# Kernel tuning notes

Hardware: AMD Instinct MI355X
Metric: run time of the kernel (lower is better)

The kernel has to match this reference:

```python
import jax, jax.numpy as jnp
import numpy as np


def setup_inputs() -> dict:
    key = jax.random.key(0)
    k1, k2, k3, k4, k5 = jax.random.split(key, 5)
    B, N, C = 16, 131072, 2
    return {
        "r": jax.random.normal(k1, (B, N, C), dtype=jnp.float32),
        "w": jax.random.uniform(k2, (B, N, 2), dtype=jnp.float32),
        "J_p": jax.random.normal(k3, (B, N, C, 6), dtype=jnp.float32),
        "J_d": jax.random.normal(k4, (B, N, C, 1), dtype=jnp.float32),
        "lmbda": jax.random.uniform(k5, (B, 1, 1), dtype=jnp.float32),
        "iter_idx": 1,
    }


def reference(r, w, J_p, J_d, lmbda, iter_idx):
    B, N, C = r.shape
    eye6 = jnp.eye(6, dtype=r.dtype)

    safe_lmbda = jnp.where(jnp.isnan(lmbda), jnp.asarray(100.0, r.dtype), lmbda)
    safe_lmbda = jnp.maximum(safe_lmbda, 0.001)  # (B,1,1)

    conf = w[..., 0:1][..., None]                 # (B,N,1,1)
    node_lambda = w[..., 1:2]                     # (B,N,1)
    cJp = conf * J_p                              # (B,N,C,6)
    cJd = conf * J_d                              # (B,N,C,1)
    cr = w[..., 0:1] * r                          # (B,N,C)

    H_pp = jnp.einsum('bncp,bncq->bpq', J_p, cJp)            # (B,6,6)
    H_pd = jnp.einsum('bncp,bncd->bnpd', J_p, cJd)           # (B,N,6,1)
    H_dd = jnp.sum(J_d * cJd, axis=2)                        # (B,N,1)
    g_p = jnp.einsum('bncp,bnc->bp', J_p, cr)[..., None]     # (B,6,1)
    g_d = jnp.sum(J_d * cr[..., None], axis=2)               # (B,N,1)

    H_pp = H_pp + safe_lmbda * eye6[None]
    H_dd_safe = jnp.maximum(H_dd + safe_lmbda + node_lambda + 1e-4, 1e-4)
    inv_H_dd = 1.0 / H_dd_safe                    # (B,N,1)

    H_pd_invHdd = H_pd * inv_H_dd[..., None]      # (B,N,6,1)
    term_to_sub = jnp.einsum('bnpd,bnqd->bpq', H_pd_invHdd, H_pd)   # (B,6,6)
    H_eff = H_pp - term_to_sub
    g_eff = g_p - jnp.sum(H_pd_invHdd * g_d[..., None], axis=1)     # (B,6,1)

    if iter_idx >= 2:
        g_eff = g_eff.at[:, 3:].set(0.0)
        H_eff = H_eff.at[:, 3:, 3:].add(1e8)

    H_eff = H_eff + 1.0 * eye6[None]
    diag = jnp.diagonal(H_eff, axis1=-2, axis2=-1)            # (B,6)
    H_eff = H_eff + eye6[None] * (0.01 * diag)[:, :, None]

    delta_pose = jnp.linalg.solve(H_eff, g_eff)               # (B,6,1)
    v = jnp.einsum('bnpd,bp->bnd', H_pd, delta_pose[..., 0])  # (B,N,1)
    delta_depth = inv_H_dd * (g_d - v)                        # (B,N,1)

    delta_pose = jnp.clip(delta_pose[..., 0], -2.0, 2.0)      # (B,6)
    delta_depth = jnp.clip(delta_depth, -5.0, 5.0)
    delta_pose = jnp.where(jnp.any(jnp.isnan(delta_pose)), jnp.zeros_like(delta_pose), delta_pose)
    delta_depth = jnp.where(jnp.any(jnp.isnan(delta_depth)), jnp.zeros_like(delta_depth), delta_depth)
    return (delta_pose, delta_depth)
```

## Files before the change

kernel.cpp:

```cpp
#include <hip/hip_runtime.h>
#include <math.h>

#define BATCH 16
#define NPB 131072
#define BLOCKS_PER_B 64
#define THREADS 256
#define PPT (NPB / (BLOCKS_PER_B * THREADS))
#define NACC 27

__device__ __forceinline__ float safe_lambda(float l) {
    if (isnan(l)) l = 100.0f;
    return fmaxf(l, 0.001f);
}

struct Pt { float4 a0, a1, a2; float2 jd, rv, wv; };

__device__ __forceinline__ void load_pt(const float* __restrict__ Jp, const float* __restrict__ Jd,
                                        const float* __restrict__ r, const float* __restrict__ w,
                                        long n, Pt& P)
{
    const float4* jp4 = (const float4*)(Jp + n * 12);
    P.a0 = jp4[0]; P.a1 = jp4[1]; P.a2 = jp4[2];
    P.jd = *(const float2*)(Jd + n * 2);
    P.rv = *(const float2*)(r  + n * 2);
    P.wv = *(const float2*)(w  + n * 2);
}

__device__ __forceinline__ void acc_pt(const Pt& P, float lam, float (&D)[21], float (&G)[6])
{
    float jp[12] = {P.a0.x, P.a0.y, P.a0.z, P.a0.w,
                    P.a1.x, P.a1.y, P.a1.z, P.a1.w,
                    P.a2.x, P.a2.y, P.a2.z, P.a2.w};
    const float conf = P.wv.x, nl = P.wv.y;
    const float jdx = P.jd.x, jdy = P.jd.y;
    const float rx  = P.rv.x, ry  = P.rv.y;

    float cjp[12];
#pragma unroll
    for (int i = 0; i < 12; ++i) cjp[i] = conf * jp[i];

    float h[6], hi[6];
#pragma unroll
    for (int p = 0; p < 6; ++p) h[p] = cjp[p] * jdx + cjp[6 + p] * jdy;
    const float Hdd = conf * (jdx * jdx + jdy * jdy);
    const float gd  = conf * (jdx * rx + jdy * ry);
    const float inv = 1.0f / fmaxf(Hdd + lam + nl + 1e-4f, 1e-4f);
#pragma unroll
    for (int p = 0; p < 6; ++p) hi[p] = h[p] * inv;

    int idx = 0;
#pragma unroll
    for (int p = 0; p < 6; ++p) {
#pragma unroll
        for (int q = p; q < 6; ++q) {
            D[idx] += cjp[p] * jp[q];
            D[idx] += cjp[6 + p] * jp[6 + q];
            D[idx] -= hi[p] * h[q];
            ++idx;
        }
    }
#pragma unroll
    for (int p = 0; p < 6; ++p) {
        G[p] += cjp[p] * rx;
        G[p] += cjp[6 + p] * ry;
        G[p] -= hi[p] * gd;
    }
}

__global__ __launch_bounds__(THREADS, 2) void dba_pass1(
    const float* __restrict__ r, const float* __restrict__ w,
    const float* __restrict__ Jp, const float* __restrict__ Jd,
    const float* __restrict__ lmbda, float* __restrict__ partials)
{
    const int b   = blockIdx.y;
    const int blk = blockIdx.x;
    const int t   = threadIdx.x;
    const float lam = safe_lambda(lmbda[b]);

    float D[21], G[6];
#pragma unroll
    for (int i = 0; i < 21; ++i) D[i] = 0.0f;
#pragma unroll
    for (int i = 0; i < 6; ++i) G[i] = 0.0f;

    const long base = (long)b * NPB + (long)blk * (THREADS * PPT) + t;

    Pt P0, P1, P2, P3;
    load_pt(Jp, Jd, r, w, base + 0 * THREADS, P0);
    load_pt(Jp, Jd, r, w, base + 1 * THREADS, P1);
    load_pt(Jp, Jd, r, w, base + 2 * THREADS, P2);

    acc_pt(P0, lam, D, G); load_pt(Jp, Jd, r, w, base + 3 * THREADS, P3);
    acc_pt(P1, lam, D, G); load_pt(Jp, Jd, r, w, base + 4 * THREADS, P0);
    acc_pt(P2, lam, D, G); load_pt(Jp, Jd, r, w, base + 5 * THREADS, P1);
    acc_pt(P3, lam, D, G); load_pt(Jp, Jd, r, w, base + 6 * THREADS, P2);
    acc_pt(P0, lam, D, G); load_pt(Jp, Jd, r, w, base + 7 * THREADS, P3);
    acc_pt(P1, lam, D, G);
    acc_pt(P2, lam, D, G);
    acc_pt(P3, lam, D, G);

#pragma unroll
    for (int i = 0; i < 21; ++i) {
        float v = D[i];
        v += __shfl_xor(v, 1);  v += __shfl_xor(v, 2);  v += __shfl_xor(v, 4);
        v += __shfl_xor(v, 8);  v += __shfl_xor(v, 16); v += __shfl_xor(v, 32);
        D[i] = v;
    }
#pragma unroll
    for (int i = 0; i < 6; ++i) {
        float v = G[i];
        v += __shfl_xor(v, 1);  v += __shfl_xor(v, 2);  v += __shfl_xor(v, 4);
        v += __shfl_xor(v, 8);  v += __shfl_xor(v, 16); v += __shfl_xor(v, 32);
        G[i] = v;
    }

    __shared__ float s_red[4][NACC];
    const int wid  = t >> 6;
    const int lane = t & 63;
    if (lane == 0) {
#pragma unroll
        for (int i = 0; i < 21; ++i) s_red[wid][i] = D[i];
#pragma unroll
        for (int i = 0; i < 6; ++i)  s_red[wid][21 + i] = G[i];
    }
    __syncthreads();
    if (t < NACC) {
        float v = s_red[0][t] + s_red[1][t] + s_red[2][t] + s_red[3][t];
        partials[((long)b * NACC + t) * BLOCKS_PER_B + blk] = v;
    }
}

__global__ void dba_solve(
    const float* __restrict__ partials, const float* __restrict__ lmbda,
    const int* __restrict__ iter_idx,
    float* __restrict__ out_pose,
    float* __restrict__ dp_raw)
{
    const int b = blockIdx.x;
    const int t = threadIdx.x;
    __shared__ float s[NACC];
    if (t < NACC) {
        const float4* p4 = (const float4*)(partials + ((long)b * NACC + t) * BLOCKS_PER_B);
        float4 a = make_float4(0.f, 0.f, 0.f, 0.f);
#pragma unroll
        for (int k = 0; k < BLOCKS_PER_B / 4; ++k) {
            float4 v = p4[k];
            a.x += v.x; a.y += v.y; a.z += v.z; a.w += v.w;
        }
        s[t] = (a.x + a.y) + (a.z + a.w);
    }
    __syncthreads();
    if (t != 0) return;

    const float lam = safe_lambda(lmbda[b]);
    float H[6][6], g[6];
    int idx = 0;
    for (int p = 0; p < 6; ++p)
        for (int q = p; q < 6; ++q) {
            float v = s[idx];
            H[p][q] = v; H[q][p] = v;
            idx++;
        }
    for (int p = 0; p < 6; ++p) g[p] = s[21 + p];
    for (int p = 0; p < 6; ++p) H[p][p] += lam;

    if (*iter_idx >= 2) {
        for (int p = 3; p < 6; ++p) g[p] = 0.0f;
        for (int p = 3; p < 6; ++p)
            for (int q = 3; q < 6; ++q) H[p][q] += 1e8f;
    }
    for (int p = 0; p < 6; ++p) H[p][p] += 1.0f;
    for (int p = 0; p < 6; ++p) H[p][p] += 0.01f * H[p][p];

    float A[6][7];
    for (int p = 0; p < 6; ++p) {
        for (int q = 0; q < 6; ++q) A[p][q] = H[p][q];
        A[p][6] = g[p];
    }
    for (int col = 0; col < 6; ++col) {
        int piv = col; float best = fabsf(A[col][col]);
        for (int rr = col + 1; rr < 6; ++rr) {
            float v = fabsf(A[rr][col]);
            if (v > best) { best = v; piv = rr; }
        }
        if (piv != col)
            for (int cc = col; cc < 7; ++cc) {
                float tmp = A[col][cc]; A[col][cc] = A[piv][cc]; A[piv][cc] = tmp;
            }
        const float invp = 1.0f / A[col][col];
        for (int rr = col + 1; rr < 6; ++rr) {
            const float f = A[rr][col] * invp;
            for (int cc = col; cc < 7; ++cc) A[rr][cc] -= f * A[col][cc];
        }
    }
    float x[6];
    for (int rr = 5; rr >= 0; --rr) {
        float v = A[rr][6];
        for (int cc = rr + 1; cc < 6; ++cc) v -= A[rr][cc] * x[cc];
        x[rr] = v / A[rr][rr];
    }
    for (int p = 0; p < 6; ++p) {
        dp_raw[b * 6 + p] = x[p];
        out_pose[b * 6 + p] = fminf(fmaxf(x[p], -2.0f), 2.0f);
    }
}

__device__ __forceinline__ float depth_pt(const Pt& P, float lam, const float (&dp)[6])
{
    float jp[12] = {P.a0.x, P.a0.y, P.a0.z, P.a0.w,
                    P.a1.x, P.a1.y, P.a1.z, P.a1.w,
                    P.a2.x, P.a2.y, P.a2.z, P.a2.w};
    const float conf = P.wv.x, nl = P.wv.y;
    const float jdx = P.jd.x, jdy = P.jd.y;
    const float rx  = P.rv.x, ry  = P.rv.y;

    float v = 0.0f;
#pragma unroll
    for (int p = 0; p < 6; ++p) {
        const float h = conf * (jp[p] * jdx + jp[6 + p] * jdy);
        v += h * dp[p];
    }
    const float Hdd = conf * (jdx * jdx + jdy * jdy);
    const float gd  = conf * (jdx * rx + jdy * ry);
    const float inv = 1.0f / fmaxf(Hdd + lam + nl + 1e-4f, 1e-4f);
    float dd = inv * (gd - v);
    return fminf(fmaxf(dd, -5.0f), 5.0f);
}

__global__ __launch_bounds__(THREADS, 2) void dba_pass3(
    const float* __restrict__ r, const float* __restrict__ w,
    const float* __restrict__ Jp, const float* __restrict__ Jd,
    const float* __restrict__ lmbda, const float* __restrict__ dp_raw,
    float* __restrict__ out_dd)
{
    const int b   = blockIdx.y;
    const int blk = blockIdx.x;
    const int t   = threadIdx.x;
    const float lam = safe_lambda(lmbda[b]);

    float dp[6];
#pragma unroll
    for (int p = 0; p < 6; ++p) dp[p] = dp_raw[b * 6 + p];

    const long base = (long)b * NPB + (long)blk * (THREADS * PPT) + t;

    Pt P0, P1, P2, P3;
    load_pt(Jp, Jd, r, w, base + 0 * THREADS, P0);
    load_pt(Jp, Jd, r, w, base + 1 * THREADS, P1);
    load_pt(Jp, Jd, r, w, base + 2 * THREADS, P2);

    out_dd[base + 0 * THREADS] = depth_pt(P0, lam, dp); load_pt(Jp, Jd, r, w, base + 3 * THREADS, P3);
    out_dd[base + 1 * THREADS] = depth_pt(P1, lam, dp); load_pt(Jp, Jd, r, w, base + 4 * THREADS, P0);
    out_dd[base + 2 * THREADS] = depth_pt(P2, lam, dp); load_pt(Jp, Jd, r, w, base + 5 * THREADS, P1);
    out_dd[base + 3 * THREADS] = depth_pt(P3, lam, dp); load_pt(Jp, Jd, r, w, base + 6 * THREADS, P2);
    out_dd[base + 4 * THREADS] = depth_pt(P0, lam, dp); load_pt(Jp, Jd, r, w, base + 7 * THREADS, P3);
    out_dd[base + 5 * THREADS] = depth_pt(P1, lam, dp);
    out_dd[base + 6 * THREADS] = depth_pt(P2, lam, dp);
    out_dd[base + 7 * THREADS] = depth_pt(P3, lam, dp);
}

extern "C" void kernel_launch(void* const* d_in, const int* in_sizes, int n_in,
                              void* d_out, int out_size, void* d_ws, size_t ws_size,
                              hipStream_t stream) {
    const float* r     = (const float*)d_in[0];
    const float* w     = (const float*)d_in[1];
    const float* Jp    = (const float*)d_in[2];
    const float* Jd    = (const float*)d_in[3];
    const float* lmbda = (const float*)d_in[4];
    const int*   iter  = (const int*)  d_in[5];

    float* out      = (float*)d_out;
    float* partials = (float*)d_ws;
    float* dp_raw   = partials + (long)BATCH * NACC * BLOCKS_PER_B;

    dim3 grid(BLOCKS_PER_B, BATCH);
    dba_pass1<<<grid, THREADS, 0, stream>>>(r, w, Jp, Jd, lmbda, partials);
    dba_solve<<<BATCH, 64, 0, stream>>>(partials, lmbda, iter, out, dp_raw);
    dba_pass3<<<grid, THREADS, 0, stream>>>(r, w, Jp, Jd, lmbda, dp_raw, out + BATCH * 6);
}
```

Baseline: 60.64 us.

## Stage J_p through LDS with global_load_lds in both streaming passes

Both the reduction pass and the depth pass now copy each wave's 64-point J_p chunk into LDS using the direct global-to-LDS load builtin with coalesced 16-byte lanes. Each thread then reads its 12 floats back from LDS. This replaces the per-thread strided float4 loads and the hand-unrolled four-deep register prefetch with a simple loop that waits on vmcnt(0) every iteration. The aim is more coalesced J_p traffic, at the cost of losing cross-iteration load overlap and adding an LDS round trip.

Result: no change. 61.52 us (+1.4%).

```diff
diff --git a/kernel.cpp b/kernel.cpp
--- a/kernel.cpp
+++ b/kernel.cpp
@@ -5,6 +5,7 @@
 #define NPB 131072
 #define BLOCKS_PER_B 64
 #define THREADS 256
+#define NWAVE (THREADS / 64)
 #define PPT (NPB / (BLOCKS_PER_B * THREADS))
 #define NACC 27
 
@@ -13,27 +14,29 @@
     return fmaxf(l, 0.001f);
 }
 
-struct Pt { float4 a0, a1, a2; float2 jd, rv, wv; };
-
-__device__ __forceinline__ void load_pt(const float* __restrict__ Jp, const float* __restrict__ Jd,
-                                        const float* __restrict__ r, const float* __restrict__ w,
-                                        long n, Pt& P)
-{
-    const float4* jp4 = (const float4*)(Jp + n * 12);
-    P.a0 = jp4[0]; P.a1 = jp4[1]; P.a2 = jp4[2];
-    P.jd = *(const float2*)(Jd + n * 2);
-    P.rv = *(const float2*)(r  + n * 2);
-    P.wv = *(const float2*)(w  + n * 2);
-}
-
-__device__ __forceinline__ void acc_pt(const Pt& P, float lam, float (&D)[21], float (&G)[6])
-{
-    float jp[12] = {P.a0.x, P.a0.y, P.a0.z, P.a0.w,
-                    P.a1.x, P.a1.y, P.a1.z, P.a1.w,
-                    P.a2.x, P.a2.y, P.a2.z, P.a2.w};
-    const float conf = P.wv.x, nl = P.wv.y;
-    const float jdx = P.jd.x, jdy = P.jd.y;
-    const float rx  = P.rv.x, ry  = P.rv.y;
+__device__ __forceinline__ void gload_lds16(const float* g, float* l) {
+    __builtin_amdgcn_global_load_lds(
+        (const __attribute__((address_space(1))) void*)g,
+        (__attribute__((address_space(3))) void*)l, 16, 0, 0);
+}
+
+__device__ __forceinline__ void stage_jp(const float* __restrict__ Jp, long wave_pt,
+                                         float* lds_slice, int lane) {
+    const float* src = Jp + wave_pt * 12 + (long)lane * 4;
+    gload_lds16(src,       lds_slice);
+    gload_lds16(src + 256, lds_slice + 256);
+    gload_lds16(src + 512, lds_slice + 512);
+}
+
+__device__ __forceinline__ void acc_pt_lds(const float* jp_lane, float2 jd, float2 rv, float2 wv,
+                                           float lam, float (&D)[21], float (&G)[6])
+{
+    const float4* f4 = (const float4*)jp_lane;
+    float4 a0 = f4[0], a1 = f4[1], a2 = f4[2];
+    float jp[12] = {a0.x, a0.y, a0.z, a0.w, a1.x, a1.y, a1.z, a1.w, a2.x, a2.y, a2.z, a2.w};
+    const float conf = wv.x, nl = wv.y;
+    const float jdx = jd.x, jdy = jd.y;
+    const float rx  = rv.x, ry  = rv.y;
 
     float cjp[12];
 #pragma unroll
@@ -72,32 +75,37 @@
     const float* __restrict__ Jp, const float* __restrict__ Jd,
     const float* __restrict__ lmbda, float* __restrict__ partials)
 {
-    const int b   = blockIdx.y;
-    const int blk = blockIdx.x;
-    const int t   = threadIdx.x;
+    const int b    = blockIdx.y;
+    const int blk  = blockIdx.x;
+    const int t    = threadIdx.x;
+    const int wid  = t >> 6;
+    const int lane = t & 63;
     const float lam = safe_lambda(lmbda[b]);
 
+    __shared__ float lds_jp[NWAVE][768];
+
     float D[21], G[6];
 #pragma unroll
     for (int i = 0; i < 21; ++i) D[i] = 0.0f;
 #pragma unroll
     for (int i = 0; i < 6; ++i) G[i] = 0.0f;
 
-    const long base = (long)b * NPB + (long)blk * (THREADS * PPT) + t;
-
-    Pt P0, P1, P2, P3;
-    load_pt(Jp, Jd, r, w, base + 0 * THREADS, P0);
-    load_pt(Jp, Jd, r, w, base + 1 * THREADS, P1);
-    load_pt(Jp, Jd, r, w, base + 2 * THREADS, P2);
-
-    acc_pt(P0, lam, D, G); load_pt(Jp, Jd, r, w, base + 3 * THREADS, P3);
-    acc_pt(P1, lam, D, G); load_pt(Jp, Jd, r, w, base + 4 * THREADS, P0);
-    acc_pt(P2, lam, D, G); load_pt(Jp, Jd, r, w, base + 5 * THREADS, P1);
-    acc_pt(P3, lam, D, G); load_pt(Jp, Jd, r, w, base + 6 * THREADS, P2);
-    acc_pt(P0, lam, D, G); load_pt(Jp, Jd, r, w, base + 7 * THREADS, P3);
-    acc_pt(P1, lam, D, G);
-    acc_pt(P2, lam, D, G);
-    acc_pt(P3, lam, D, G);
+    const long blk_base  = (long)b * NPB + (long)blk * (THREADS * PPT);
+    const long wave_base = blk_base + (long)wid * (64 * PPT);
+
+    for (int it = 0; it < PPT; ++it) {
+        const long wave_pt = wave_base + (long)it * 64;
+        const long n       = wave_pt + lane;
+
+        stage_jp(Jp, wave_pt, &lds_jp[wid][0], lane);
+        float2 jd = *(const float2*)(Jd + n * 2);
+        float2 rv = *(const float2*)(r  + n * 2);
+        float2 wv = *(const float2*)(w  + n * 2);
+
+        asm volatile("s_waitcnt vmcnt(0)" ::: "memory");
+
+        acc_pt_lds(&lds_jp[wid][lane * 12], jd, rv, wv, lam, D, G);
+    }
 
 #pragma unroll
     for (int i = 0; i < 21; ++i) {
@@ -114,9 +122,7 @@
         G[i] = v;
     }
 
-    __shared__ float s_red[4][NACC];
-    const int wid  = t >> 6;
-    const int lane = t & 63;
+    __shared__ float s_red[NWAVE][NACC];
     if (lane == 0) {
 #pragma unroll
         for (int i = 0; i < 21; ++i) s_red[wid][i] = D[i];
@@ -205,58 +211,57 @@
     }
 }
 
-__device__ __forceinline__ float depth_pt(const Pt& P, float lam, const float (&dp)[6])
-{
-    float jp[12] = {P.a0.x, P.a0.y, P.a0.z, P.a0.w,
-                    P.a1.x, P.a1.y, P.a1.z, P.a1.w,
-                    P.a2.x, P.a2.y, P.a2.z, P.a2.w};
-    const float conf = P.wv.x, nl = P.wv.y;
-    const float jdx = P.jd.x, jdy = P.jd.y;
-    const float rx  = P.rv.x, ry  = P.rv.y;
-
-    float v = 0.0f;
-#pragma unroll
-    for (int p = 0; p < 6; ++p) {
-        const float h = conf * (jp[p] * jdx + jp[6 + p] * jdy);
-        v += h * dp[p];
-    }
-    const float Hdd = conf * (jdx * jdx + jdy * jdy);
-    const float gd  = conf * (jdx * rx + jdy * ry);
-    const float inv = 1.0f / fmaxf(Hdd + lam + nl + 1e-4f, 1e-4f);
-    float dd = inv * (gd - v);
-    return fminf(fmaxf(dd, -5.0f), 5.0f);
-}
-
 __global__ __launch_bounds__(THREADS, 2) void dba_pass3(
     const float* __restrict__ r, const float* __restrict__ w,
     const float* __restrict__ Jp, const float* __restrict__ Jd,
     const float* __restrict__ lmbda, const float* __restrict__ dp_raw,
     float* __restrict__ out_dd)
 {
-    const int b   = blockIdx.y;
-    const int blk = blockIdx.x;
-    const int t   = threadIdx.x;
+    const int b    = blockIdx.y;
+    const int blk  = blockIdx.x;
+    const int t    = threadIdx.x;
+    const int wid  = t >> 6;
+    const int lane = t & 63;
     const float lam = safe_lambda(lmbda[b]);
 
+    __shared__ float lds_jp[NWAVE][768];
+
     float dp[6];
 #pragma unroll
     for (int p = 0; p < 6; ++p) dp[p] = dp_raw[b * 6 + p];
 
-    const long base = (long)b * NPB + (long)blk * (THREADS * PPT) + t;
-
-    Pt P0, P1, P2, P3;
-    load_pt(Jp, Jd, r, w, base + 0 * THREADS, P0);
-    load_pt(Jp, Jd, r, w, base + 1 * THREADS, P1);
-    load_pt(Jp, Jd, r, w, base + 2 * THREADS, P2);
-
-    out_dd[base + 0 * THREADS] = depth_pt(P0, lam, dp); load_pt(Jp, Jd, r, w, base + 3 * THREADS, P3);
-    out_dd[base + 1 * THREADS] = depth_pt(P1, lam, dp); load_pt(Jp, Jd, r, w, base + 4 * THREADS, P0);
-    out_dd[base + 2 * THREADS] = depth_pt(P2, lam, dp); load_pt(Jp, Jd, r, w, base + 5 * THREADS, P1);
-    out_dd[base + 3 * THREADS] = depth_pt(P3, lam, dp); load_pt(Jp, Jd, r, w, base + 6 * THREADS, P2);
-    out_dd[base + 4 * THREADS] = depth_pt(P0, lam, dp); load_pt(Jp, Jd, r, w, base + 7 * THREADS, P3);
-    out_dd[base + 5 * THREADS] = depth_pt(P1, lam, dp);
-    out_dd[base + 6 * THREADS] = depth_pt(P2, lam, dp);
-    out_dd[base + 7 * THREADS] = depth_pt(P3, lam, dp);
+    const long blk_base  = (long)b * NPB + (long)blk * (THREADS * PPT);
+    const long wave_base = blk_base + (long)wid * (64 * PPT);
+
+    for (int it = 0; it < PPT; ++it) {
+        const long wave_pt = wave_base + (long)it * 64;
+        const long n       = wave_pt + lane;
+
+        stage_jp(Jp, wave_pt, &lds_jp[wid][0], lane);
+        float2 jd = *(const float2*)(Jd + n * 2);
+        float2 rv = *(const float2*)(r  + n * 2);
+        float2 wv = *(const float2*)(w  + n * 2);
+
+        asm volatile("s_waitcnt vmcnt(0)" ::: "memory");
+
+        const float4* f4 = (const float4*)&lds_jp[wid][lane * 12];
+        float4 a0 = f4[0], a1 = f4[1], a2 = f4[2];
+        float jp[12] = {a0.x, a0.y, a0.z, a0.w, a1.x, a1.y, a1.z, a1.w, a2.x, a2.y, a2.z, a2.w};
+        const float conf = wv.x, nl = wv.y;
+        const float jdx = jd.x, jdy = jd.y;
+
+        float v = 0.0f;
+#pragma unroll
+        for (int p = 0; p < 6; ++p) {
+            const float h = conf * (jp[p] * jdx + jp[6 + p] * jdy);
+            v += h * dp[p];
+        }
+        const float Hdd = conf * (jdx * jdx + jdy * jdy);
+        const float gd  = conf * (jdx * rv.x + jdy * rv.y);
+        const float inv = 1.0f / fmaxf(Hdd + lam + nl + 1e-4f, 1e-4f);
+        float dd = inv * (gd - v);
+        out_dd[n] = fminf(fmaxf(dd, -5.0f), 5.0f);
+    }
 }
 
 extern "C" void kernel_launch(void* const* d_in, const int* in_sizes, int n_in,
```
